# Kernel tuning notes

Measured on AMD Instinct MI355X. Metric: run time of the kernel, lower is better.

The kernel has to match this reference:

```python
import jax, jax.numpy as jnp
import numpy as np

T, B, C = 4, 2, 128
LT, LH, LW = 8, 32, 32
NUM_HEADS = 8
HEAD_DIM = C // NUM_HEADS
THETA = 0.7
V_TH = 1.0
TAU = 2.0  # spikingjelly LIFNode default tau
N_WIN = (2, 2, 2)
TOPK = 4
EPS = 1e-5
ATAN_ALPHA = 2.0  # spikingjelly surrogate.ATan default


@jax.custom_vjp
def spike(x):
    return (x >= 0.0).astype(x.dtype)

def _spike_fwd(x):
    return spike(x), x

def _spike_bwd(x, g):
    s = (jnp.pi / 2.0) * ATAN_ALPHA * x
    return (g * (ATAN_ALPHA / 2.0) / (1.0 + s * s),)

spike.defvjp(_spike_fwd, _spike_bwd)


def lif(x_seq):
    """Multi-step LIF: v'=v+(x-v)/tau, spike at v>=V_TH, hard reset to 0 (detached)."""
    def step(v, x):
        v = v + (x - v) / TAU
        s = spike(v - V_TH)
        v = v * (1.0 - jax.lax.stop_gradient(s))  # detach_reset, v_reset=0
        return v, s
    _, s_seq = jax.lax.scan(step, jnp.zeros_like(x_seq[0]), x_seq)
    return s_seq


def bn(x, gamma, beta):
    # BatchNorm3d(track_running_stats=False) on [T*B, C, D, H, W]: batch stats per channel
    mean = x.mean(axis=(0, 1, 3, 4, 5), keepdims=True)
    var = x.var(axis=(0, 1, 3, 4, 5), keepdims=True)
    shp = (1, 1, -1, 1, 1, 1)
    return (x - mean) * jax.lax.rsqrt(var + EPS) * gamma.reshape(shp) + beta.reshape(shp)


def conv3d(x, w, pad):
    t, b = x.shape[:2]
    y = jax.lax.conv_general_dilated(
        x.reshape((t * b,) + x.shape[2:]), w,
        window_strides=(1, 1, 1), padding=[(pad, pad)] * 3,
        dimension_numbers=('NCDHW', 'OIDHW', 'NCDHW'))
    return y.reshape((t, b) + y.shape[1:])


def cdc_t(x, w):
    out = conv3d(x, w, 1)
    # central-difference temporal term: 1x1x1 conv with summed first/last temporal slices
    kd = w[:, :, 0].sum((-1, -2)) + w[:, :, 2].sum((-1, -2))  # [O, I]
    return out - THETA * jnp.einsum('oi,tbidhw->tbodhw', kd, x)


def to_wins(t):
    wt, wh, ww = N_WIN
    Tn, Bn, Cn, Lt, Lh, Lw = t.shape
    lt, lh, lw = Lt // wt, Lh // wh, Lw // ww
    t = t.reshape(Tn, Bn, Cn, wt, lt, wh, lh, ww, lw)
    t = t.transpose(0, 1, 3, 5, 7, 4, 6, 8, 2)
    return t.reshape(Tn, Bn, wt * wh * ww, lt * lh * lw, Cn)


def setup_inputs() -> dict:
    key = jax.random.key(0)
    ks = jax.random.split(key, 4)
    x = jax.random.normal(ks[0], (T, B, C, LT, LH, LW), jnp.float32)
    qw = jax.random.normal(ks[1], (C, C, 3, 3, 3), jnp.float32) / np.sqrt(C * 27)
    kw = jax.random.normal(ks[2], (C, C), jnp.float32) / np.sqrt(C)
    pw = jax.random.normal(ks[3], (C, C), jnp.float32) / np.sqrt(C)
    ones = jnp.ones((C,), jnp.float32)
    zeros = jnp.zeros((C,), jnp.float32)
    return {"x": x, "qw": qw, "q_gamma": ones, "q_beta": zeros,
            "kw": kw, "k_gamma": ones, "k_beta": zeros,
            "v_gamma": ones, "v_beta": zeros,
            "pw": pw, "p_gamma": ones, "p_beta": zeros}


def reference(x, qw, q_gamma, q_beta, kw, k_gamma, k_beta,
              v_gamma, v_beta, pw, p_gamma, p_beta):
    Tn, Bn, Cn, Lt, Lh, Lw = x.shape
    wt, wh, ww = N_WIN
    num_wins = wt * wh * ww
    lt, lh, lw = Lt // wt, Lh // wh, Lw // ww

    q_real = bn(cdc_t(x, qw), q_gamma, q_beta)
    k_real = bn(jnp.einsum('oi,tbidhw->tbodhw', kw, x), k_gamma, k_beta)

    # region-level routing from pre-spike activations
    q_region = to_wins(q_real).mean(axis=(0, 3))  # [B, W, C]
    k_region = to_wins(k_real).mean(axis=(0, 3))
    a_r = jnp.einsum('bwc,bvc->bwv', q_region, k_region) * (HEAD_DIM ** -0.5)
    k_eff = min(TOPK, num_wins)
    _, idx = jax.lax.top_k(a_r, k_eff)  # [B, W, k]

    q = lif(q_real)
    k = lif(k_real)
    v = lif(bn(x, v_gamma, v_beta))
    q_w = to_wins(q)  # [T,B,W,S,C]
    k_w = to_wins(k)
    v_w = to_wins(v)

    # gather routed windows per (batch, target window), mean-aggregate over top-k
    gather = jax.vmap(lambda src_b, idx_b: src_b[:, idx_b], in_axes=(1, 0), out_axes=1)
    k_agg = gather(k_w, idx).mean(axis=3)  # [T,B,W,S,C]
    v_agg = gather(v_w, idx).mean(axis=3)

    S = q_w.shape[3]
    q_h = q_w.reshape(Tn, Bn, num_wins, S, NUM_HEADS, HEAD_DIM)
    k_h = k_agg.reshape(Tn, Bn, num_wins, S, NUM_HEADS, HEAD_DIM)
    v_h = v_agg.reshape(Tn, Bn, num_wins, S, NUM_HEADS, HEAD_DIM)

    attn = (q_h * k_h).sum(axis=5, keepdims=True)  # [T,B,W,S,H,1]
    attn = lif(attn)
    out = (attn * v_h).reshape(Tn, Bn, num_wins, S, Cn)

    out = out.reshape(Tn, Bn, wt, wh, ww, lt, lh, lw, Cn)
    out = out.transpose(0, 1, 8, 2, 5, 3, 6, 4, 7).reshape(Tn, Bn, Cn, Lt, Lh, Lw)

    out = lif(out)
    out = bn(jnp.einsum('oi,tbidhw->tbodhw', pw, out), p_gamma, p_beta)
    return out
```

## Files before the change

### kernel.cpp

```cpp
#include <hip/hip_runtime.h>

#define TT 4
#define BB 2
#define CC 128
#define DD 8
#define HHH 32
#define WWW 32
#define PP (DD*HHH*WWW)
#define TSTRIDE (BB*CC*PP)
#define NWIN 8
#define SSS 1024
#define NHEAD 8
#define HDIM 16
#define THETA 0.7f
#define VTH 1.0f
#define NPERC (TT*BB*PP)
#define EPSf 1e-5f

typedef unsigned short ushortT;
typedef unsigned char ucharT;
typedef _Float16 half_t;
typedef _Float16 f16x8 __attribute__((ext_vector_type(8)));
typedef float    f32x16 __attribute__((ext_vector_type(16)));

typedef const __attribute__((address_space(1))) void* as1_cvp;
typedef __attribute__((address_space(3))) void* as3_vp;

__global__ __launch_bounds__(256) void prep_wmodT(const float* __restrict__ qw,
                                                  float* __restrict__ wmodT) {
    int oi = blockIdx.x*256 + threadIdx.x;
    if (oi >= CC*CC) return;
    int o  = oi >> 7;
    int ic = oi & 127;
    const float* wp = qw + (size_t)oi*27;
    float kd = 0.f;
    #pragma unroll
    for (int t=0; t<9; t++) kd += wp[t] + wp[18+t];
    #pragma unroll
    for (int t=0; t<27; t++) {
        float v = wp[t] - ((t==13) ? THETA*kd : 0.f);
        wmodT[((size_t)o*27 + t)*CC + ic] = v;
    }
}

__global__ __launch_bounds__(256) void prep_wfrag(const float* __restrict__ wmodT,
                                                  half_t* __restrict__ wfrag) {
    int id = blockIdx.x*256 + threadIdx.x;
    if (id >= 8*27*4*64) return;
    int lane = id & 63;
    int r = id >> 6;
    int m = r & 3; r >>= 2;
    int t = r % 27;
    int kb = r / 27;
    int o   = m*32 + (lane & 31);
    int ic0 = kb*16 + (lane>>5)*8;
    size_t base = ((size_t)(id>>6))*2*64*8 + (size_t)lane*8;
    #pragma unroll
    for (int j=0;j<8;j++){
        float v = wmodT[((size_t)o*27 + t)*CC + ic0 + j];
        half_t h = (half_t)v;
        half_t l = (half_t)(v - (float)h);
        wfrag[base + 0*64*8 + j] = h;
        wfrag[base + 1*64*8 + j] = l;
    }
}

__global__ __launch_bounds__(256) void prep_w1frag2(const float* __restrict__ Wk,
                                                    const float* __restrict__ Wp,
                                                    half_t* __restrict__ fragk,
                                                    half_t* __restrict__ fragp) {
    int id = blockIdx.x*256 + threadIdx.x;
    if (id >= 4096) return;
    const float* W    = (id < 2048) ? Wk : Wp;
    half_t*      frag = (id < 2048) ? fragk : fragp;
    int i2 = id & 2047;
    int lane = i2 & 63;
    int r = i2 >> 6;
    int m = r & 3;
    int kb = r >> 2;
    int o   = m*32 + (lane & 31);
    int ic0 = kb*16 + (lane>>5)*8;
    size_t base = ((size_t)(kb*4+m))*2*64*8 + (size_t)lane*8;
    #pragma unroll
    for (int j=0;j<8;j++){
        float v = W[(size_t)o*CC + ic0 + j];
        half_t h = (half_t)v;
        half_t l = (half_t)(v - (float)h);
        frag[base + 0*64*8 + j] = h;
        frag[base + 1*64*8 + j] = l;
    }
}

__global__ __launch_bounds__(256) void build_xsplit(const float* __restrict__ x,
                                                    half_t* __restrict__ xsp) {
    int id = blockIdx.x*256 + threadIdx.x;
    if (id >= 8*16*8*34*34) return;
    int wt = id % 34; int r = id/34;
    int hp = r % 34;  r /= 34;
    int dz = r % 8;   r /= 8;
    int icg = r & 15; int tb = r >> 4;
    bool inb = (hp>=1) & (hp<=32) & (wt>=1) & (wt<=32);
    half_t h8[8], l8[8];
    #pragma unroll
    for (int j=0;j<8;j++){
        float v = 0.f;
        if (inb)
            v = x[((size_t)(tb*CC + icg*8+j))*PP + (size_t)dz*1024 + (hp-1)*32 + (wt-1)];
        half_t h = (half_t)v;
        half_t l = (half_t)(v - (float)h);
        h8[j]=h; l8[j]=l;
    }
    #pragma unroll
    for (int sp=0; sp<2; sp++){
        size_t gu = (((((size_t)tb*2 + sp)*16 + icg)*8 + dz)*34 + hp)*34 + wt;
        half_t* dst = xsp + gu*8;
        const half_t* src = (sp==0)?h8:l8;
        #pragma unroll
        for (int j=0;j<8;j++) dst[j] = src[j];
    }
}

__global__ __launch_bounds__(512,2) void conv_mfma3(const half_t* __restrict__ xsp,
                                                    const half_t* __restrict__ wfrag,
                                                    float* __restrict__ y0,
                                                    float* __restrict__ y1) {
    extern __shared__ half_t slab[];
    int tid  = threadIdx.x;
    int wid  = tid >> 6;
    int lane = tid & 63;
    int ln   = lane & 31;
    int half_ = lane >> 5;
    int hg = blockIdx.x;
    int dp = blockIdx.y;
    int z  = blockIdx.z;
    int tb = z >> 1, kh = z & 1;
    int H0 = hg*4, d0 = dp*4;
    int r  = wid & 3;
    int mh = wid >> 2;
    float* y = kh ? y1 : y0;

    auto STAGE = [&](int bk, int bsel) {
        int kb = kh*4 + bk;
        half_t* bufp = slab + (size_t)bsel*(4896*8);
        #pragma unroll 1
        for (int k2=0; k2<10; k2++) {
            int u = tid + (k2<<9);
            if (u < 4896) {
                int sp  = (u >= 2448) ? 1 : 0;
                int r1  = u - sp*2448;
                int icg = (r1 >= 1224) ? 1 : 0;
                int p2  = r1 - icg*1224;
                int dzs = p2/204; int r3 = p2 - dzs*204;
                int hp  = r3/34;  int wt = r3 - hp*34;
                int dd  = d0 - 1 + dzs;
                const half_t* src = ((unsigned)dd < 8u)
                    ? &xsp[((((((size_t)tb*2 + sp)*16 + (kb*2+icg))*8 + dd)*34 + (H0+hp))*34 + wt)*8]
                    : &xsp[(size_t)ln*8];
                __builtin_amdgcn_global_load_lds((as1_cvp)src,
                    (as3_vp)(bufp + (size_t)u*8), 16, 0, 0);
            }
        }
    };

    f32x16 acc[4][2];
    #pragma unroll
    for (int dt=0;dt<4;dt++)
        #pragma unroll
        for (int mm=0;mm<2;mm++)
            #pragma unroll
            for (int i=0;i<16;i++) acc[dt][mm][i] = 0.f;

    f16x8 ca[2][2];
    #pragma unroll
    for (int mm=0;mm<2;mm++)
        #pragma unroll
        for (int sp=0;sp<2;sp++)
            ca[mm][sp] = *(const f16x8*)&wfrag[((((size_t)(kh*4*27)*4 + (mh*2+mm))*2+sp)*64 + lane)*8];

    asm volatile("" ::: "memory");
    STAGE(0,0);
    STAGE(1,1);
    asm volatile("" ::: "memory");

    #pragma unroll 1
    for (int kk=0; kk<4; kk++) {
        int kb = kh*4 + kk;
        if (kk == 0) {
            if (wid < 5) asm volatile("s_waitcnt vmcnt(10)" ::: "memory");
            else         asm volatile("s_waitcnt vmcnt(9)"  ::: "memory");
        } else {
            asm volatile("s_waitcnt vmcnt(63)" ::: "memory");
        }
        __builtin_amdgcn_s_barrier();
        asm volatile("" ::: "memory");
        const half_t* bufp = slab + (size_t)(kk&1)*(4896*8);

        f16x8 cbX[2][2], cbY[2][2];
        #pragma unroll
        for (int dt=0; dt<2; dt++){
            int unitb = dt*204 + r*34 + ln;
            #pragma unroll
            for (int sp=0; sp<2; sp++)
                cbX[dt][sp] = *(const f16x8*)&bufp[(size_t)((sp*2+half_)*1224 + unitb)*8];
        }

        #pragma unroll 1
        for (int t=0; t<27; t++) {
            int dz=t/9; int rr=t-dz*9; int dh=rr/3; int dw=rr-dh*3;
            #pragma unroll
            for (int dt=0; dt<2; dt++){
                int unitb = (dt+2 + dz)*204 + (r+dh)*34 + (ln+dw);
                #pragma unroll
                for (int sp=0; sp<2; sp++)
                    cbY[dt][sp] = *(const f16x8*)&bufp[(size_t)((sp*2+half_)*1224 + unitb)*8];
            }
            f16x8 na[2][2];
            int nt  = (t<26)? t+1 : 0;
            int nkb = (t<26)? kb  : ((kk<3)? kb+1 : kb);
            #pragma unroll
            for (int mm=0;mm<2;mm++)
                #pragma unroll
                for (int sp=0;sp<2;sp++)
                    na[mm][sp] = *(const f16x8*)&wfrag[((((size_t)(nkb*27+nt)*4+(mh*2+mm))*2+sp)*64 + lane)*8];
            #pragma unroll
            for (int dt=0;dt<2;dt++)
                #pragma unroll
                for (int mm=0;mm<2;mm++) acc[dt][mm] = __builtin_amdgcn_mfma_f32_32x32x16_f16(ca[mm][0], cbX[dt][0], acc[dt][mm],0,0,0);
            #pragma unroll
            for (int dt=0;dt<2;dt++)
                #pragma unroll
                for (int mm=0;mm<2;mm++) acc[dt][mm] = __builtin_amdgcn_mfma_f32_32x32x16_f16(ca[mm][0], cbX[dt][1], acc[dt][mm],0,0,0);
            #pragma unroll
            for (int dt=0;dt<2;dt++)
                #pragma unroll
                for (int mm=0;mm<2;mm++) acc[dt][mm] = __builtin_amdgcn_mfma_f32_32x32x16_f16(ca[mm][1], cbX[dt][0], acc[dt][mm],0,0,0);
            {
                int t2 = (t<26)? t+1 : 26;
                int dz2=t2/9; int rr2=t2-dz2*9; int dh2=rr2/3; int dw2=rr2-dh2*3;
                #pragma unroll
                for (int dt=0; dt<2; dt++){
                    int unitb = (dt + dz2)*204 + (r+dh2)*34 + (ln+dw2);
                    #pragma unroll
                    for (int sp=0; sp<2; sp++)
                        cbX[dt][sp] = *(const f16x8*)&bufp[(size_t)((sp*2+half_)*1224 + unitb)*8];
                }
            }
            #pragma unroll
            for (int dt=0;dt<2;dt++)
                #pragma unroll
                for (int mm=0;mm<2;mm++) acc[dt+2][mm] = __builtin_amdgcn_mfma_f32_32x32x16_f16(ca[mm][0], cbY[dt][0], acc[dt+2][mm],0,0,0);
            #pragma unroll
            for (int dt=0;dt<2;dt++)
                #pragma unroll
                for (int mm=0;mm<2;mm++) acc[dt+2][mm] = __builtin_amdgcn_mfma_f32_32x32x16_f16(ca[mm][0], cbY[dt][1], acc[dt+2][mm],0,0,0);
            #pragma unroll
            for (int dt=0;dt<2;dt++)
                #pragma unroll
                for (int mm=0;mm<2;mm++) acc[dt+2][mm] = __builtin_amdgcn_mfma_f32_32x32x16_f16(ca[mm][1], cbY[dt][0], acc[dt+2][mm],0,0,0);
            #pragma unroll
            for (int mm=0;mm<2;mm++)
                #pragma unroll
                for (int sp=0;sp<2;sp++) ca[mm][sp] = na[mm][sp];
        }
        asm volatile("" ::: "memory");
        __builtin_amdgcn_s_barrier();
        asm volatile("" ::: "memory");
        if (kk < 2) STAGE(kk+2, kk&1);
    }

    int h = H0 + r;
    #pragma unroll
    for (int dt=0; dt<4; dt++) {
        int d = d0 + dt;
        #pragma unroll
        for (int mm=0; mm<2; mm++) {
            #pragma unroll
            for (int reg=0; reg<16; reg++) {
                int row = (reg&3) + 8*(reg>>2) + 4*half_;
                int o = (mh*2+mm)*32 + row;
                y[((size_t)tb*CC + o)*PP + d*1024 + h*32 + ln] = acc[dt][mm][reg];
            }
        }
    }
}

__global__ __launch_bounds__(256) void kgemm_mfma(const half_t* __restrict__ xsp,
                                                  const half_t* __restrict__ wk,
                                                  float* __restrict__ y) {
    int tid  = threadIdx.x;
    int wid  = tid >> 6;
    int lane = tid & 63;
    int ln   = lane & 31;
    int half_ = lane >> 5;
    int hg = blockIdx.x, d = blockIdx.y, tb = blockIdx.z;
    int h = hg*4 + wid;

    f32x16 acc[4];
    #pragma unroll
    for (int m=0;m<4;m++)
        #pragma unroll
        for (int i=0;i<16;i++) acc[m][i] = 0.f;

    #pragma unroll 2
    for (int kb=0; kb<8; kb++) {
        f16x8 b[2];
        #pragma unroll
        for (int sp=0; sp<2; sp++) {
            size_t gu = (((((size_t)tb*2 + sp)*16 + (kb*2+half_))*8 + d)*34 + (h+1))*34 + (ln+1);
            b[sp] = *(const f16x8*)&xsp[gu*8];
        }
        #pragma unroll
        for (int m=0; m<4; m++) {
            const half_t* wb = wk + ((size_t)(kb*4+m))*2*64*8 + (size_t)lane*8;
            f16x8 a0 = *(const f16x8*)&wb[0*64*8];
            f16x8 a1 = *(const f16x8*)&wb[1*64*8];
            acc[m] = __builtin_amdgcn_mfma_f32_32x32x16_f16(a0, b[0], acc[m],0,0,0);
            acc[m] = __builtin_amdgcn_mfma_f32_32x32x16_f16(a0, b[1], acc[m],0,0,0);
            acc[m] = __builtin_amdgcn_mfma_f32_32x32x16_f16(a1, b[0], acc[m],0,0,0);
        }
    }
    #pragma unroll
    for (int m=0; m<4; m++) {
        #pragma unroll
        for (int reg=0; reg<16; reg++) {
            int row = (reg&3) + 8*(reg>>2) + 4*half_;
            int o = m*32 + row;
            y[((size_t)tb*CC + o)*PP + d*1024 + h*32 + ln] = acc[m][reg];
        }
    }
}

__global__ __launch_bounds__(256) void pgemm_mfma(const ushortT* __restrict__ spkb,
                                                  const half_t* __restrict__ wp,
                                                  float* __restrict__ y) {
    int tid  = threadIdx.x;
    int wid  = tid >> 6;
    int lane = tid & 63;
    int ln   = lane & 31;
    int half_ = lane >> 5;
    int hg = blockIdx.x, d = blockIdx.y, tb = blockIdx.z;
    int h = hg*4 + wid;
    int p = d*1024 + h*32 + ln;

    f32x16 acc[4];
    #pragma unroll
    for (int m=0;m<4;m++)
        #pragma unroll
        for (int i=0;i<16;i++) acc[m][i] = 0.f;

    #pragma unroll 2
    for (int kb=0; kb<8; kb++) {
        f16x8 b = *(const f16x8*)&spkb[(((size_t)tb*16 + (kb*2+half_))*PP + p)*8];
        #pragma unroll
        for (int m=0; m<4; m++) {
            const half_t* wb = wp + ((size_t)(kb*4+m))*2*64*8 + (size_t)lane*8;
            f16x8 a0 = *(const f16x8*)&wb[0*64*8];
            f16x8 a1 = *(const f16x8*)&wb[1*64*8];
            acc[m] = __builtin_amdgcn_mfma_f32_32x32x16_f16(a0, b, acc[m],0,0,0);
            acc[m] = __builtin_amdgcn_mfma_f32_32x32x16_f16(a1, b, acc[m],0,0,0);
        }
    }
    #pragma unroll
    for (int m=0; m<4; m++) {
        #pragma unroll
        for (int reg=0; reg<16; reg++) {
            int row = (reg&3) + 8*(reg>>2) + 4*half_;
            int o = m*32 + row;
            y[((size_t)tb*CC + o)*PP + p] = acc[m][reg];
        }
    }
}

__global__ __launch_bounds__(128) void win_stats(const float* __restrict__ q0,
        const float* __restrict__ q1,
        const float* __restrict__ k, const float* __restrict__ x,
        float* __restrict__ rsum, float* __restrict__ rsq) {
    int blk = blockIdx.x;
    int src = blk >> 11;
    int r   = blk & 2047;
    const float* base = (src==0) ? q0 : ((src==1) ? k : x);
    int c  = r & 127;
    int wi = (r >> 7) & 7;
    int b  = r >> 10;
    int wd = wi>>2, wh = (wi>>1)&1, ww = wi&1;
    int tid = threadIdx.x;
    float s=0.f, s2=0.f;
    for (int t=0;t<TT;t++){
        size_t off0 = ((size_t)(t*BB+b)*CC + c)*PP;
        const float* p  = base + off0;
        const float* p2 = q1 + off0;
        for (int si=tid; si<SSS; si+=128){
            int ld = si>>8, lh=(si>>4)&15, lw=si&15;
            int o = ((wd*4+ld)<<10) + ((wh*16+lh)<<5) + (ww*16+lw);
            float v = p[o];
            if (src==0) v += p2[o];
            s += v; s2 += v*v;
        }
    }
    __shared__ float ls[128], ls2[128];
    ls[tid]=s; ls2[tid]=s2; __syncthreads();
    for (int off=64;off>0;off>>=1){
        if(tid<off){ ls[tid]+=ls[tid+off]; ls2[tid]+=ls2[tid+off]; }
        __syncthreads();
    }
    if (tid==0){ rsum[blk]=ls[0]; rsq[blk]=ls2[0]; }
}

__global__ __launch_bounds__(384) void route_fin(const float* __restrict__ rsum,
        const float* __restrict__ rsq,
        const float* __restrict__ qg, const float* __restrict__ qb,
        const float* __restrict__ kg, const float* __restrict__ kb,
        float* __restrict__ stats, int* __restrict__ idxout) {
    __shared__ float qn[16*128], kn[16*128], ar[16*8];
    __shared__ float csum[384], csq[384];
    int tid = threadIdx.x;
    {
        int src = tid >> 7, c = tid & 127;
        float s=0.f, s2=0.f;
        for (int bw=0; bw<16; bw++){
            int idx = src*2048 + bw*128 + c;
            s  += rsum[idx];
            s2 += rsq[idx];
        }
        stats[src*256 + c]       = s;
        stats[src*256 + 128 + c] = s2;
        csum[tid]=s; csq[tid]=s2;
    }
    __syncthreads();
    for (int e=tid; e<16*128; e+=384){
        int c = e&127;
        float qm = csum[c]*(1.f/NPERC);
        float qv = csq[c]*(1.f/NPERC) - qm*qm;
        float qr = rsqrtf(qv + EPSf);
        qn[e] = (rsum[e]*(1.f/(TT*SSS)) - qm)*qr*qg[c] + qb[c];
        float km = csum[128+c]*(1.f/NPERC);
        float kv = csq[128+c]*(1.f/NPERC) - km*km;
        float kr = rsqrtf(kv + EPSf);
        kn[e] = (rsum[2048+e]*(1.f/(TT*SSS)) - km)*kr*kg[c] + kb[c];
    }
    __syncthreads();
    if (tid < 128){
        int b = tid>>6, w=(tid>>3)&7, v=tid&7;
        float s=0.f;
        for (int c=0;c<128;c++) s += qn[(b*8+w)*128+c]*kn[(b*8+v)*128+c];
        ar[(b*8+w)*8+v] = s * 0.25f;
    }
    __syncthreads();
    if (tid < 16){
        const float* row = &ar[tid*8];
        bool used[8] = {false,false,false,false,false,false,false,false};
        for (int j=0;j<4;j++){
            int best=0; float bv=-3.0e38f;
            for (int v=0; v<8; v++){
                if (!used[v] && row[v] > bv){ bv=row[v]; best=v; }
            }
            used[best]=true;
            idxout[tid*4+j]=best;
        }
    }
}

__global__ __launch_bounds__(256) void lif_bn_win3(const float* __restrict__ q0,
        const float* __restrict__ q1,
        const float* __restrict__ kin, const float* __restrict__ xin,
        ucharT* __restrict__ qs, ucharT* __restrict__ ks, ucharT* __restrict__ vs,
        const float* __restrict__ stats,
        const float* __restrict__ qg, const float* __restrict__ qb,
        const float* __restrict__ kg, const float* __restrict__ kb,
        const float* __restrict__ vg, const float* __restrict__ vb) {
    int src = blockIdx.y;
    const float* in  = (src==0) ? q0 : ((src==1) ? kin : xin);
    ucharT*      spk = (src==0) ? qs  : ((src==1) ? ks  : vs);
    const float* gamma = (src==0) ? qg : ((src==1) ? kg : vg);
    const float* beta  = (src==0) ? qb : ((src==1) ? kb : vb);
    int e = blockIdx.x*256 + threadIdx.x;
    if (e >= BB*CC*PP) return;
    int p = e & (PP-1);
    int c = (e >> 13) & 127;
    int b = e >> 20;
    float mean = stats[src*256 + c]*(1.f/NPERC);
    float var  = stats[src*256 + 128 + c]*(1.f/NPERC) - mean*mean;
    float sc = rsqrtf(var+EPSf)*gamma[c];
    float sh = beta[c] - mean*sc;
    int d = p>>10, h=(p>>5)&31, w=p&31;
    int wi = ((d>>2)*2 + (h>>4))*2 + (w>>4);
    int si = (((d&3)<<4) + (h&15))*16 + (w&15);
    size_t widx = ((size_t)(b*NWIN+wi)*CC + c)*SSS + si;
    float v=0.f;
    #pragma unroll
    for (int t=0;t<TT;t++){
        size_t ti = (size_t)t*TSTRIDE + e;
        float raw = in[ti];
        if (src==0) raw += q1[ti];
        float xn = raw*sc + sh;
        v = (v+xn)*0.5f;
        float s = (v>=VTH)?1.f:0.f;
        spk[(size_t)t*TSTRIDE + widx] = (ucharT)(v>=VTH ? 1 : 0);
        v *= (1.f - s);
    }
}

__global__ __launch_bounds__(256) void attn_lif(const ucharT* __restrict__ qspk,
        const ucharT* __restrict__ kspk, const ucharT* __restrict__ vspk,
        const int* __restrict__ idx, ushortT* __restrict__ spkb) {
    int id = blockIdx.x*256 + threadIdx.x;
    if (id >= BB*NWIN*NHEAD*SSS) return;
    int s  = id & 1023;
    int hh = (id>>10) & 7;
    int wi = (id>>13) & 7;
    int b  = id>>16;
    int bw = b*NWIN+wi;
    size_t qbase = ((size_t)bw*CC + hh*HDIM)*SSS + s;
    size_t sbase[4];
    #pragma unroll
    for (int j=0;j<4;j++){
        int src = idx[bw*4+j];
        sbase[j] = ((size_t)(b*NWIN+src)*CC + hh*HDIM)*SSS + s;
    }
    int wd = wi>>2, wh = (wi>>1)&1, ww = wi&1;
    int d3 = wd*4 + (s>>8), h3 = wh*16 + ((s>>4)&15), w3 = ww*16 + (s&15);
    int p  = (d3<<10) + (h3<<5) + w3;

    float v=0.f;
    float v2[16];
    #pragma unroll
    for (int dd=0; dd<16; dd++) v2[dd]=0.f;

    #pragma unroll 1
    for (int t=0;t<TT;t++){
        size_t toff = (size_t)t*TSTRIDE;
        int km[16], vm[16];
        #pragma unroll
        for (int dd=0;dd<16;dd++){ km[dd]=0; vm[dd]=0; }
        #pragma unroll
        for (int j=0;j<4;j++){
            const ucharT* kp = kspk+toff+sbase[j];
            const ucharT* vp = vspk+toff+sbase[j];
            #pragma unroll
            for (int dd=0; dd<16; dd++){
                km[dd] += kp[(size_t)dd*SSS];
                vm[dd] += vp[(size_t)dd*SSS];
            }
        }
        const ucharT* qp = qspk+toff+qbase;
        int atti=0;
        #pragma unroll
        for (int dd=0;dd<16;dd++) atti += (int)qp[(size_t)dd*SSS]*km[dd];
        float att = (float)atti * 0.25f;
        v = (v+att)*0.5f;
        float sp = (v>=VTH)?1.f:0.f;
        v *= (1.f-sp);
        float spq = sp*0.25f;
        union { ushortT u[8]; uint4 q4; } pk0, pk1;
        #pragma unroll
        for (int dd=0;dd<16;dd++){
            float ov = spq*(float)vm[dd];
            v2[dd] = (v2[dd]+ov)*0.5f;
            float s2 = (v2[dd]>=VTH)?1.f:0.f;
            v2[dd] *= (1.f-s2);
            ushortT bs = (s2 != 0.f) ? (ushortT)0x3C00 : (ushortT)0;
            if (dd < 8) pk0.u[dd] = bs; else pk1.u[dd-8] = bs;
        }
        int tb2 = t*BB + b;
        size_t base = (((size_t)tb2*16 + hh*2)*PP + p)*8;
        *(uint4*)&spkb[base] = pk0.q4;
        *(uint4*)&spkb[base + (size_t)PP*8] = pk1.q4;
    }
}

__global__ __launch_bounds__(256) void pstats_part(const float* __restrict__ xin,
        float* __restrict__ part_sum, float* __restrict__ part_sq) {
    int blk = blockIdx.x;
    int c = blk & 127, tb = blk >> 7;
    int tid = threadIdx.x;
    const float* p = xin + ((size_t)tb*CC + c)*PP;
    float s=0.f, s2=0.f;
    for (int i=tid; i<PP; i+=256){ float v=p[i]; s+=v; s2+=v*v; }
    __shared__ float ls[256], ls2[256];
    ls[tid]=s; ls2[tid]=s2; __syncthreads();
    for (int off=128; off>0; off>>=1){
        if (tid<off){ ls[tid]+=ls[tid+off]; ls2[tid]+=ls2[tid+off]; }
        __syncthreads();
    }
    if (tid==0){ part_sum[blk]=ls[0]; part_sq[blk]=ls2[0]; }
}

__global__ __launch_bounds__(256) void bn_apply(const float* __restrict__ xin,
        float* __restrict__ yout,
        const float* __restrict__ part_sum, const float* __restrict__ part_sq,
        const float* __restrict__ gamma, const float* __restrict__ beta) {
    size_t i = (size_t)blockIdx.x*256 + threadIdx.x;
    if (i >= (size_t)TT*BB*CC*PP) return;
    int c = (int)((i>>13)&127);
    float s=0.f, s2=0.f;
    #pragma unroll
    for (int tb=0; tb<8; tb++){
        s  += part_sum[tb*128+c];
        s2 += part_sq[tb*128+c];
    }
    float mean = s*(1.f/NPERC);
    float var  = s2*(1.f/NPERC) - mean*mean;
    float sc = rsqrtf(var+EPSf)*gamma[c];
    float sh = beta[c] - mean*sc;
    yout[i] = xin[i]*sc + sh;
}

extern "C" void kernel_launch(void* const* d_in, const int* in_sizes, int n_in,
                              void* d_out, int out_size, void* d_ws, size_t ws_size,
                              hipStream_t stream) {
    const float* x  = (const float*)d_in[0];
    const float* qw = (const float*)d_in[1];
    const float* qg = (const float*)d_in[2];
    const float* qb = (const float*)d_in[3];
    const float* kw = (const float*)d_in[4];
    const float* kg = (const float*)d_in[5];
    const float* kb = (const float*)d_in[6];
    const float* vg = (const float*)d_in[7];
    const float* vb = (const float*)d_in[8];
    const float* pw = (const float*)d_in[9];
    const float* pg = (const float*)d_in[10];
    const float* pb = (const float*)d_in[11];
    float* out = (float*)d_out;
    float* ws  = (float*)d_ws;

    const size_t NEL = (size_t)TT*TSTRIDE;
    float* part0 = ws;
    float* part1 = ws + NEL;
    half_t* xsp  = (half_t*)(ws + 2*NEL);
    const size_t KCONV_OFF = 2*NEL + 10747904;
    float* kconv = ws + KCONV_OFF;
    float* wf_base = ws + KCONV_OFF + NEL;
    half_t* wfrag  = (half_t*)wf_base;
    half_t* wkfrag = (half_t*)(wf_base + 442368);
    float*  wmodT  = wf_base + 442368 + 16384;
    half_t* wpfrag = (half_t*)(wf_base + 442368 + 16384 + 442368);
    float* stats = ws + 5*NEL;
    float* rsum = stats + 1024;
    float* rsq  = rsum + 6144;
    float* ppart_sum = rsq + 6144;
    float* ppart_sq  = ppart_sum + 1024;
    int*   idxp = (int*)(ppart_sq + 1024);

    ucharT* qspk = (ucharT*)(ws + 2*NEL);
    ucharT* kspk = (ucharT*)(ws + 2*NEL) + 8388608;
    ucharT* vspk = (ucharT*)(ws + 2*NEL) + 16777216;
    ushortT* spkb  = (ushortT*)ws;
    float*  pconv  = ws + KCONV_OFF;

    prep_wmodT<<<64,256,0,stream>>>(qw, wmodT);
    prep_wfrag<<<216,256,0,stream>>>(wmodT, wfrag);
    prep_w1frag2<<<16,256,0,stream>>>(kw, pw, wkfrag, wpfrag);
    build_xsplit<<<4624,256,0,stream>>>(x, xsp);
    {
        static bool attr_set = false;
        const int shmem = 2*4896*8*(int)sizeof(half_t);
        if (!attr_set) {
            hipFuncSetAttribute((const void*)conv_mfma3,
                                hipFuncAttributeMaxDynamicSharedMemorySize, shmem);
            attr_set = true;
        }
        dim3 cg(8,2,16);
        conv_mfma3<<<cg,512,shmem,stream>>>(xsp, wfrag, part0, part1);
    }
    {
        dim3 gg(8,8,8);
        kgemm_mfma<<<gg,256,0,stream>>>(xsp, wkfrag, kconv);
    }
    win_stats<<<6144,128,0,stream>>>(part0, part1, kconv, x, rsum, rsq);
    route_fin<<<1,384,0,stream>>>(rsum, rsq, qg,qb,kg,kb, stats, idxp);
    {
        dim3 lg(8192,3);
        lif_bn_win3<<<lg,256,0,stream>>>(part0,part1,kconv,x,
                                         qspk,kspk,vspk,
                                         stats, qg,qb,kg,kb,vg,vb);
    }
    attn_lif<<<512,256,0,stream>>>(qspk,kspk,vspk,idxp,spkb);
    {
        dim3 gg(8,8,8);
        pgemm_mfma<<<gg,256,0,stream>>>(spkb, wpfrag, pconv);
    }
    pstats_part<<<1024,256,0,stream>>>(pconv, ppart_sum, ppart_sq);
    bn_apply<<<32768,256,0,stream>>>(pconv, out, ppart_sum, ppart_sq, pg, pb);
}
```

Measured before the change: 392.4 us.

## Replace split-K conv partials with full-K per block over fewer depth slices

The 3x3x3 conv kernel no longer splits the input-channel reduction across two blocks writing separate partial outputs. Each block now covers all 8 channel groups but only 2 depth slices instead of 4, with a smaller shared slab, and accumulates into two register sets that are summed at store time. Downstream stats and LIF kernels read a single conv output instead of adding two partial buffers, which removes an extra full-size write and read. The trade-off is less halo reuse per block (2 depth outputs per 4 staged slices), a longer serial K loop per block, and fewer MFMAs between LDS fragment loads.

```diff
diff --git a/kernel.cpp b/kernel.cpp
--- a/kernel.cpp
+++ b/kernel.cpp
@@ -120,10 +120,9 @@
     }
 }
 
-__global__ __launch_bounds__(512,2) void conv_mfma3(const half_t* __restrict__ xsp,
+__global__ __launch_bounds__(512,2) void conv_mfma4(const half_t* __restrict__ xsp,
                                                     const half_t* __restrict__ wfrag,
-                                                    float* __restrict__ y0,
-                                                    float* __restrict__ y1) {
+                                                    float* __restrict__ y) {
     extern __shared__ half_t slab[];
     int tid  = threadIdx.x;
     int wid  = tid >> 6;
@@ -132,24 +131,21 @@
     int half_ = lane >> 5;
     int hg = blockIdx.x;
     int dp = blockIdx.y;
-    int z  = blockIdx.z;
-    int tb = z >> 1, kh = z & 1;
-    int H0 = hg*4, d0 = dp*4;
+    int tb = blockIdx.z;
+    int H0 = hg*4, d0 = dp*2;
     int r  = wid & 3;
     int mh = wid >> 2;
-    float* y = kh ? y1 : y0;
-
-    auto STAGE = [&](int bk, int bsel) {
-        int kb = kh*4 + bk;
-        half_t* bufp = slab + (size_t)bsel*(4896*8);
+
+    auto STAGE = [&](int kb, int bsel) {
+        half_t* bufp = slab + (size_t)bsel*(3264*8);
         #pragma unroll 1
-        for (int k2=0; k2<10; k2++) {
+        for (int k2=0; k2<7; k2++) {
             int u = tid + (k2<<9);
-            if (u < 4896) {
-                int sp  = (u >= 2448) ? 1 : 0;
-                int r1  = u - sp*2448;
-                int icg = (r1 >= 1224) ? 1 : 0;
-                int p2  = r1 - icg*1224;
+            if (u < 3264) {
+                int sp  = (u >= 1632) ? 1 : 0;
+                int r1  = u - sp*1632;
+                int icg = (r1 >= 816) ? 1 : 0;
+                int p2  = r1 - icg*816;
                 int dzs = p2/204; int r3 = p2 - dzs*204;
                 int hp  = r3/34;  int wt = r3 - hp*34;
                 int dd  = d0 - 1 + dzs;
@@ -162,61 +158,60 @@
         }
     };
 
-    f32x16 acc[4][2];
-    #pragma unroll
-    for (int dt=0;dt<4;dt++)
+    f32x16 accA[2][2], accB[2][2];
+    #pragma unroll
+    for (int dt=0;dt<2;dt++)
         #pragma unroll
         for (int mm=0;mm<2;mm++)
             #pragma unroll
-            for (int i=0;i<16;i++) acc[dt][mm][i] = 0.f;
+            for (int i=0;i<16;i++){ accA[dt][mm][i]=0.f; accB[dt][mm][i]=0.f; }
 
     f16x8 ca[2][2];
     #pragma unroll
     for (int mm=0;mm<2;mm++)
         #pragma unroll
         for (int sp=0;sp<2;sp++)
-            ca[mm][sp] = *(const f16x8*)&wfrag[((((size_t)(kh*4*27)*4 + (mh*2+mm))*2+sp)*64 + lane)*8];
+            ca[mm][sp] = *(const f16x8*)&wfrag[((((size_t)0*4 + (mh*2+mm))*2+sp)*64 + lane)*8];
 
     asm volatile("" ::: "memory");
     STAGE(0,0);
     STAGE(1,1);
     asm volatile("" ::: "memory");
 
-    #pragma unroll 1
-    for (int kk=0; kk<4; kk++) {
-        int kb = kh*4 + kk;
+    auto KBODY = [&](int kk, f32x16 (&acc)[2][2]) {
         if (kk == 0) {
-            if (wid < 5) asm volatile("s_waitcnt vmcnt(10)" ::: "memory");
-            else         asm volatile("s_waitcnt vmcnt(9)"  ::: "memory");
+            if (wid < 3) asm volatile("s_waitcnt vmcnt(7)" ::: "memory");
+            else         asm volatile("s_waitcnt vmcnt(6)" ::: "memory");
         } else {
             asm volatile("s_waitcnt vmcnt(63)" ::: "memory");
         }
         __builtin_amdgcn_s_barrier();
         asm volatile("" ::: "memory");
-        const half_t* bufp = slab + (size_t)(kk&1)*(4896*8);
-
-        f16x8 cbX[2][2], cbY[2][2];
+        const half_t* bufp = slab + (size_t)(kk&1)*(3264*8);
+
+        f16x8 cbC[2][2], cbN[2][2];
         #pragma unroll
         for (int dt=0; dt<2; dt++){
             int unitb = dt*204 + r*34 + ln;
             #pragma unroll
             for (int sp=0; sp<2; sp++)
-                cbX[dt][sp] = *(const f16x8*)&bufp[(size_t)((sp*2+half_)*1224 + unitb)*8];
+                cbC[dt][sp] = *(const f16x8*)&bufp[(size_t)((sp*2+half_)*816 + unitb)*8];
         }
 
         #pragma unroll 1
         for (int t=0; t<27; t++) {
-            int dz=t/9; int rr=t-dz*9; int dh=rr/3; int dw=rr-dh*3;
+            int t2 = (t<26)? t+1 : 26;
+            int dz2=t2/9; int rr2=t2-dz2*9; int dh2=rr2/3; int dw2=rr2-dh2*3;
             #pragma unroll
             for (int dt=0; dt<2; dt++){
-                int unitb = (dt+2 + dz)*204 + (r+dh)*34 + (ln+dw);
+                int unitb = (dt + dz2)*204 + (r+dh2)*34 + (ln+dw2);
                 #pragma unroll
                 for (int sp=0; sp<2; sp++)
-                    cbY[dt][sp] = *(const f16x8*)&bufp[(size_t)((sp*2+half_)*1224 + unitb)*8];
+                    cbN[dt][sp] = *(const f16x8*)&bufp[(size_t)((sp*2+half_)*816 + unitb)*8];
             }
             f16x8 na[2][2];
             int nt  = (t<26)? t+1 : 0;
-            int nkb = (t<26)? kb  : ((kk<3)? kb+1 : kb);
+            int nkb = (t<26)? kk  : ((kk<7)? kk+1 : kk);
             #pragma unroll
             for (int mm=0;mm<2;mm++)
                 #pragma unroll
@@ -225,38 +220,19 @@
             #pragma unroll
             for (int dt=0;dt<2;dt++)
                 #pragma unroll
-                for (int mm=0;mm<2;mm++) acc[dt][mm] = __builtin_amdgcn_mfma_f32_32x32x16_f16(ca[mm][0], cbX[dt][0], acc[dt][mm],0,0,0);
+                for (int mm=0;mm<2;mm++) acc[dt][mm] = __builtin_amdgcn_mfma_f32_32x32x16_f16(ca[mm][0], cbC[dt][0], acc[dt][mm],0,0,0);
             #pragma unroll
             for (int dt=0;dt<2;dt++)
                 #pragma unroll
-                for (int mm=0;mm<2;mm++) acc[dt][mm] = __builtin_amdgcn_mfma_f32_32x32x16_f16(ca[mm][0], cbX[dt][1], acc[dt][mm],0,0,0);
+                for (int mm=0;mm<2;mm++) acc[dt][mm] = __builtin_amdgcn_mfma_f32_32x32x16_f16(ca[mm][0], cbC[dt][1], acc[dt][mm],0,0,0);
             #pragma unroll
             for (int dt=0;dt<2;dt++)
                 #pragma unroll
-                for (int mm=0;mm<2;mm++) acc[dt][mm] = __builtin_amdgcn_mfma_f32_32x32x16_f16(ca[mm][1], cbX[dt][0], acc[dt][mm],0,0,0);
-            {
-                int t2 = (t<26)? t+1 : 26;
-                int dz2=t2/9; int rr2=t2-dz2*9; int dh2=rr2/3; int dw2=rr2-dh2*3;
-                #pragma unroll
-                for (int dt=0; dt<2; dt++){
-                    int unitb = (dt + dz2)*204 + (r+dh2)*34 + (ln+dw2);
-                    #pragma unroll
-                    for (int sp=0; sp<2; sp++)
-                        cbX[dt][sp] = *(const f16x8*)&bufp[(size_t)((sp*2+half_)*1224 + unitb)*8];
-                }
-            }
+                for (int mm=0;mm<2;mm++) acc[dt][mm] = __builtin_amdgcn_mfma_f32_32x32x16_f16(ca[mm][1], cbC[dt][0], acc[dt][mm],0,0,0);
             #pragma unroll
             for (int dt=0;dt<2;dt++)
                 #pragma unroll
-                for (int mm=0;mm<2;mm++) acc[dt+2][mm] = __builtin_amdgcn_mfma_f32_32x32x16_f16(ca[mm][0], cbY[dt][0], acc[dt+2][mm],0,0,0);
-            #pragma unroll
-            for (int dt=0;dt<2;dt++)
-                #pragma unroll
-                for (int mm=0;mm<2;mm++) acc[dt+2][mm] = __builtin_amdgcn_mfma_f32_32x32x16_f16(ca[mm][0], cbY[dt][1], acc[dt+2][mm],0,0,0);
-            #pragma unroll
-            for (int dt=0;dt<2;dt++)
-                #pragma unroll
-                for (int mm=0;mm<2;mm++) acc[dt+2][mm] = __builtin_amdgcn_mfma_f32_32x32x16_f16(ca[mm][1], cbY[dt][0], acc[dt+2][mm],0,0,0);
+                for (int sp=0;sp<2;sp++) cbC[dt][sp] = cbN[dt][sp];
             #pragma unroll
             for (int mm=0;mm<2;mm++)
                 #pragma unroll
@@ -265,12 +241,17 @@
         asm volatile("" ::: "memory");
         __builtin_amdgcn_s_barrier();
         asm volatile("" ::: "memory");
-        if (kk < 2) STAGE(kk+2, kk&1);
-    }
+        if (kk < 6) STAGE(kk+2, kk&1);
+    };
+
+    #pragma unroll 1
+    for (int kk=0; kk<4; kk++) KBODY(kk, accA);
+    #pragma unroll 1
+    for (int kk=4; kk<8; kk++) KBODY(kk, accB);
 
     int h = H0 + r;
     #pragma unroll
-    for (int dt=0; dt<4; dt++) {
+    for (int dt=0; dt<2; dt++) {
         int d = d0 + dt;
         #pragma unroll
         for (int mm=0; mm<2; mm++) {
@@ -278,7 +259,8 @@
             for (int reg=0; reg<16; reg++) {
                 int row = (reg&3) + 8*(reg>>2) + 4*half_;
                 int o = (mh*2+mm)*32 + row;
-                y[((size_t)tb*CC + o)*PP + d*1024 + h*32 + ln] = acc[dt][mm][reg];
+                y[((size_t)tb*CC + o)*PP + d*1024 + h*32 + ln]
+                    = accA[dt][mm][reg] + accB[dt][mm][reg];
             }
         }
     }
@@ -371,14 +353,13 @@
     }
 }
 
-__global__ __launch_bounds__(128) void win_stats(const float* __restrict__ q0,
-        const float* __restrict__ q1,
+__global__ __launch_bounds__(128) void win_stats(const float* __restrict__ q,
         const float* __restrict__ k, const float* __restrict__ x,
         float* __restrict__ rsum, float* __restrict__ rsq) {
     int blk = blockIdx.x;
     int src = blk >> 11;
     int r   = blk & 2047;
-    const float* base = (src==0) ? q0 : ((src==1) ? k : x);
+    const float* base = (src==0) ? q : ((src==1) ? k : x);
     int c  = r & 127;
     int wi = (r >> 7) & 7;
     int b  = r >> 10;
@@ -386,14 +367,10 @@
     int tid = threadIdx.x;
     float s=0.f, s2=0.f;
     for (int t=0;t<TT;t++){
-        size_t off0 = ((size_t)(t*BB+b)*CC + c)*PP;
-        const float* p  = base + off0;
-        const float* p2 = q1 + off0;
+        const float* p = base + ((size_t)(t*BB+b)*CC + c)*PP;
         for (int si=tid; si<SSS; si+=128){
             int ld = si>>8, lh=(si>>4)&15, lw=si&15;
-            int o = ((wd*4+ld)<<10) + ((wh*16+lh)<<5) + (ww*16+lw);
-            float v = p[o];
-            if (src==0) v += p2[o];
+            float v = p[((wd*4+ld)<<10) + ((wh*16+lh)<<5) + (ww*16+lw)];
             s += v; s2 += v*v;
         }
     }
@@ -460,8 +437,7 @@
     }
 }
 
-__global__ __launch_bounds__(256) void lif_bn_win3(const float* __restrict__ q0,
-        const float* __restrict__ q1,
+__global__ __launch_bounds__(256) void lif_bn_win3(const float* __restrict__ qin,
         const float* __restrict__ kin, const float* __restrict__ xin,
         ucharT* __restrict__ qs, ucharT* __restrict__ ks, ucharT* __restrict__ vs,
         const float* __restrict__ stats,
@@ -469,7 +445,7 @@
         const float* __restrict__ kg, const float* __restrict__ kb,
         const float* __restrict__ vg, const float* __restrict__ vb) {
     int src = blockIdx.y;
-    const float* in  = (src==0) ? q0 : ((src==1) ? kin : xin);
+    const float* in  = (src==0) ? qin : ((src==1) ? kin : xin);
     ucharT*      spk = (src==0) ? qs  : ((src==1) ? ks  : vs);
     const float* gamma = (src==0) ? qg : ((src==1) ? kg : vg);
     const float* beta  = (src==0) ? qb : ((src==1) ? kb : vb);
@@ -489,10 +465,7 @@
     float v=0.f;
     #pragma unroll
     for (int t=0;t<TT;t++){
-        size_t ti = (size_t)t*TSTRIDE + e;
-        float raw = in[ti];
-        if (src==0) raw += q1[ti];
-        float xn = raw*sc + sh;
+        float xn = in[(size_t)t*TSTRIDE + e]*sc + sh;
         v = (v+xn)*0.5f;
         float s = (v>=VTH)?1.f:0.f;
         spk[(size_t)t*TSTRIDE + widx] = (ucharT)(v>=VTH ? 1 : 0);
@@ -624,8 +597,7 @@
     float* ws  = (float*)d_ws;
 
     const size_t NEL = (size_t)TT*TSTRIDE;
-    float* part0 = ws;
-    float* part1 = ws + NEL;
+    float* qconv = ws;
     half_t* xsp  = (half_t*)(ws + 2*NEL);
     const size_t KCONV_OFF = 2*NEL + 10747904;
     float* kconv = ws + KCONV_OFF;
@@ -653,24 +625,24 @@
     build_xsplit<<<4624,256,0,stream>>>(x, xsp);
     {
         static bool attr_set = false;
-        const int shmem = 2*4896*8*(int)sizeof(half_t);
+        const int shmem = 2*3264*8*(int)sizeof(half_t);
         if (!attr_set) {
-            hipFuncSetAttribute((const void*)conv_mfma3,
+            hipFuncSetAttribute((const void*)conv_mfma4,
                                 hipFuncAttributeMaxDynamicSharedMemorySize, shmem);
             attr_set = true;
         }
-        dim3 cg(8,2,16);
-        conv_mfma3<<<cg,512,shmem,stream>>>(xsp, wfrag, part0, part1);
+        dim3 cg(8,4,8);
+        conv_mfma4<<<cg,512,shmem,stream>>>(xsp, wfrag, qconv);
     }
     {
         dim3 gg(8,8,8);
         kgemm_mfma<<<gg,256,0,stream>>>(xsp, wkfrag, kconv);
     }
-    win_stats<<<6144,128,0,stream>>>(part0, part1, kconv, x, rsum, rsq);
+    win_stats<<<6144,128,0,stream>>>(qconv, kconv, x, rsum, rsq);
     route_fin<<<1,384,0,stream>>>(rsum, rsq, qg,qb,kg,kb, stats, idxp);
     {
         dim3 lg(8192,3);
-        lif_bn_win3<<<lg,256,0,stream>>>(part0,part1,kconv,x,
+        lif_bn_win3<<<lg,256,0,stream>>>(qconv,kconv,x,
                                          qspk,kspk,vspk,
                                          stats, qg,qb,kg,kb,vg,vb);
     }
```

New measurement: 390.4 us. About the same (-0.5%).
